# Kernel optimization log

Hardware: AMD Instinct MI355X
Metric: run time of the kernel (lower is better)

The kernel has to match this reference:

```python
import jax, jax.numpy as jnp
import numpy as np

N_NODES = 200000
H_DIM = 64
OUT_DIM = 32
NUM_RELS = 8
NUM_BASES = 8
N_EDGES = 1000000


def setup_inputs() -> dict:
    key = jax.random.key(0)
    ks = jax.random.split(key, 10)
    emb = jax.random.normal(ks[0], (N_NODES, H_DIM), dtype=jnp.float32) * 0.1
    basis1 = jax.random.normal(ks[1], (NUM_BASES, H_DIM, H_DIM), dtype=jnp.float32) * 0.05
    comp1 = jax.random.normal(ks[2], (NUM_RELS, NUM_BASES), dtype=jnp.float32)
    bias1 = jnp.zeros((H_DIM,), dtype=jnp.float32)
    basis2 = jax.random.normal(ks[3], (NUM_BASES, H_DIM, OUT_DIM), dtype=jnp.float32) * 0.05
    comp2 = jax.random.normal(ks[4], (NUM_RELS, NUM_BASES), dtype=jnp.float32)
    bias2 = jnp.zeros((OUT_DIM,), dtype=jnp.float32)
    src = jax.random.randint(ks[5], (N_EDGES,), 0, N_NODES, dtype=jnp.int32)
    dst = jax.random.randint(ks[6], (N_EDGES,), 0, N_NODES, dtype=jnp.int32)
    etype = jax.random.randint(ks[7], (N_EDGES,), 0, NUM_RELS, dtype=jnp.int32)
    norm = jax.random.uniform(ks[8], (N_EDGES, 1), dtype=jnp.float32)
    return {"emb": emb, "basis1": basis1, "comp1": comp1, "bias1": bias1,
            "basis2": basis2, "comp2": comp2, "bias2": bias2,
            "src": src, "dst": dst, "etype": etype, "norm": norm}


def _rel_graph_conv(x, basis, comp, bias, src, dst, etype, norm, num_nodes):
    # basis regularizer: W_r = sum_b comp[r,b] * basis[b]  -> [R, in, out]
    W = jnp.einsum('rb,bio->rio', comp, basis)
    # transform all nodes under every relation: [R, N, out]
    y = jnp.einsum('ni,rio->rno', x, W)
    # per-edge message: gather transformed src feature for the edge's relation
    msg = y[etype, src] * norm  # [E, out]
    # scatter-sum to destination nodes
    agg = jax.ops.segment_sum(msg, dst, num_segments=num_nodes)
    return agg + bias


def reference(emb, basis1, comp1, bias1, basis2, comp2, bias2, src, dst, etype, norm):
    h = _rel_graph_conv(emb, basis1, comp1, bias1, src, dst, etype, norm, emb.shape[0])
    h = _rel_graph_conv(h, basis2, comp2, bias2, src, dst, etype, norm, emb.shape[0])
    return h
```

## Files before the change

### kernel.cpp

```cpp
#include <hip/hip_runtime.h>
#include <hip/hip_bf16.h>

#define NRELS 8
#define NB 8
#define PBLK 256
#define BSH 9
#define BCAP 3584

typedef __attribute__((ext_vector_type(8))) short short8v;
typedef __attribute__((ext_vector_type(4))) float f32x4;

__device__ __forceinline__ short bfc(float f) {
    __hip_bfloat16 h = __float2bfloat16(f);
    return *reinterpret_cast<short*>(&h);
}
__device__ __forceinline__ float bf2f(ushort u) {
    return __uint_as_float((unsigned)u << 16);
}

__global__ void wprep_kernel(const float* __restrict__ basis1, const float* __restrict__ comp1,
                             const float* __restrict__ basis2, const float* __restrict__ comp2,
                             short* __restrict__ Wf1, short* __restrict__ Wf2) {
    int idx = blockIdx.x * blockDim.x + threadIdx.x;
    const int n1 = 16 * 4 * 64 * 8;
    const int n2 = 16 * 2 * 64 * 8;
    if (idx < n1) {
        int j = idx & 7, lane = (idx >> 3) & 63, nt = (idx >> 9) & 3, ks = idx >> 11;
        int k512 = ks * 32 + (lane >> 4) * 8 + j;
        int r = k512 >> 6, k64 = k512 & 63;
        int c = nt * 16 + (lane & 15);
        float s = 0.f;
#pragma unroll
        for (int b = 0; b < NB; ++b)
            s = fmaf(comp1[r * NB + b], basis1[b * 4096 + k64 * 64 + c], s);
        Wf1[idx] = bfc(s);
    } else if (idx < n1 + n2) {
        int i2 = idx - n1;
        int j = i2 & 7, lane = (i2 >> 3) & 63, nt = (i2 >> 9) & 1, ks = i2 >> 10;
        int k512 = ks * 32 + (lane >> 4) * 8 + j;
        int r = k512 >> 6, k64 = k512 & 63;
        int c = nt * 16 + (lane & 15);
        float s = 0.f;
#pragma unroll
        for (int b = 0; b < NB; ++b)
            s = fmaf(comp2[r * NB + b], basis2[b * 2048 + k64 * 32 + c], s);
        Wf2[i2] = bfc(s);
    }
}

__global__ void cvt_kernel(const float* __restrict__ in, ushort* __restrict__ outb, int n4) {
    for (int i = blockIdx.x * blockDim.x + threadIdx.x; i < n4;
         i += gridDim.x * blockDim.x) {
        float4 v = reinterpret_cast<const float4*>(in)[i];
        ushort4 o;
        o.x = (ushort)bfc(v.x); o.y = (ushort)bfc(v.y);
        o.z = (ushort)bfc(v.z); o.w = (ushort)bfc(v.w);
        reinterpret_cast<ushort4*>(outb)[i] = o;
    }
}

__global__ void histA_kernel(const int* __restrict__ dst, int* __restrict__ histM,
                             int nEdges, int nBuck, int chunk) {
    __shared__ int h[512];
    for (int t = threadIdx.x; t < nBuck; t += 256) h[t] = 0;
    __syncthreads();
    int start = blockIdx.x * chunk;
    int end = min(nEdges, start + chunk);
    for (int i = start + threadIdx.x; i < end; i += 256)
        atomicAdd(&h[dst[i] >> BSH], 1);
    __syncthreads();
    for (int t = threadIdx.x; t < nBuck; t += 256)
        histM[t * PBLK + blockIdx.x] = h[t];
}

__global__ void scanA_kernel(const int* __restrict__ histM, int* __restrict__ offs,
                             int* __restrict__ bucketBase, int nBuck, int nBlk, int nEdges) {
    __shared__ int tot[512];
    const int b = threadIdx.x;
    int s = 0;
    if (b < nBuck) {
        const int4* hp = (const int4*)(histM + b * nBlk);
        for (int k = 0; k < nBlk / 4; ++k) {
            int4 v = hp[k];
            s += v.x + v.y + v.z + v.w;
        }
    }
    tot[b] = s;
    __syncthreads();
    int own = s;
    for (int st = 1; st < 512; st <<= 1) {
        int t = (b >= st) ? tot[b - st] : 0;
        __syncthreads();
        tot[b] += t;
        __syncthreads();
    }
    int base = tot[b] - own;
    if (b < nBuck) {
        bucketBase[b] = base;
        int run = base;
        const int4* hp = (const int4*)(histM + b * nBlk);
        int4* op = (int4*)(offs + b * nBlk);
        for (int k = 0; k < nBlk / 4; ++k) {
            int4 h4 = hp[k];
            int4 o4;
            o4.x = run; run += h4.x;
            o4.y = run; run += h4.y;
            o4.z = run; run += h4.z;
            o4.w = run; run += h4.w;
            op[k] = o4;
        }
    }
    if (b == 0) bucketBase[nBuck] = nEdges;
}

__global__ void part_kernel(const int* __restrict__ src, const int* __restrict__ dst,
                            const int* __restrict__ et, const float* __restrict__ norm,
                            const int* __restrict__ offs, uint2* __restrict__ staged,
                            int nEdges, int nBuck, int chunk) {
    __shared__ int cur[512];
    for (int t = threadIdx.x; t < nBuck; t += 256)
        cur[t] = offs[t * PBLK + blockIdx.x];
    __syncthreads();
    int start = blockIdx.x * chunk;
    int end = min(nEdges, start + chunk);
    for (int i = start + threadIdx.x; i < end; i += 256) {
        int d = dst[i];
        int b = d >> BSH;
        int p = atomicAdd(&cur[b], 1);
        staged[p] = make_uint2(((unsigned)(d & 511) << 21) |
                               ((unsigned)src[i] << 3) | (unsigned)et[i],
                               __float_as_uint(norm[i]));
    }
}

__global__ void sortB_kernel(uint2* __restrict__ meta, const int* __restrict__ bucketBase,
                             int* __restrict__ endOff, int nNodes) {
    const int b = blockIdx.x;
    const int tid = threadIdx.x;
    const int e0 = bucketBase[b];
    const int n = min(bucketBase[b + 1] - e0, BCAP);
    __shared__ uint2 st[BCAP];
    __shared__ int h[4352];
    __shared__ int pb[256];
#pragma unroll
    for (int k = 0; k < 16; ++k) h[tid * 17 + k] = 0;
    __syncthreads();
    for (int j = tid; j < n; j += 256) {
        uint2 v = meta[e0 + j];
        st[j] = v;
        int key = (int)((v.x >> 21) << 3) | (int)(v.x & 7u);
        atomicAdd(&h[key + (key >> 4)], 1);
    }
    __syncthreads();
    int loc[16];
    int s = 0;
#pragma unroll
    for (int k = 0; k < 16; ++k) { loc[k] = h[tid * 17 + k]; s += loc[k]; }
    pb[tid] = s;
    __syncthreads();
    for (int stp = 1; stp < 256; stp <<= 1) {
        int t = (tid >= stp) ? pb[tid - stp] : 0;
        __syncthreads();
        pb[tid] += t;
        __syncthreads();
    }
    int run = pb[tid] - s;
    const int d0 = b << BSH;
#pragma unroll
    for (int k = 0; k < 16; ++k) {
        h[tid * 17 + k] = run;
        run += loc[k];
        if ((k & 7) == 7) {
            int d = d0 + tid * 2 + (k >> 3);
            if (d < nNodes) endOff[d] = e0 + run;
        }
    }
    __syncthreads();
    for (int j = tid; j < n; j += 256) {
        uint2 v = st[j];
        int key = (int)((v.x >> 21) << 3) | (int)(v.x & 7u);
        int r = atomicAdd(&h[key + (key >> 4)], 1);
        meta[e0 + r] = make_uint2(v.x & 0x1FFFFFu, v.y);
    }
}

template <int OUT, typename OutT>
__global__ __launch_bounds__(256, 4) void fused_kernel(
    const ushort* __restrict__ xb, const short* __restrict__ Wf,
    const uint2* __restrict__ meta, const int* __restrict__ endOff,
    const float* __restrict__ bias, OutT* __restrict__ out, int nNodes) {
    constexpr int NT = OUT / 16;
    __shared__ ushort ab[16][520];
    const int lane = threadIdx.x & 63;
    const int wslot = threadIdx.x >> 6;
    const int d0blk = blockIdx.x * 16;
    const int d0 = d0blk + wslot * 4;
    const int rowBase = wslot * 4;

    {
        ushort4 z4 = {0, 0, 0, 0};
#pragma unroll
        for (int r = 0; r < 4; ++r) {
            *(ushort4*)&ab[rowBase + r][lane * 4] = z4;
            *(ushort4*)&ab[rowBase + r][256 + lane * 4] = z4;
        }
    }

    if (d0 < nNodes) {
        const int d1 = min(d0 + 4, nNodes);
        int bndv = 0x7fffffff;
        if (lane < 4) bndv = endOff[min(d0 + lane, nNodes - 1)];
        const int eEnd = __builtin_amdgcn_readlane(bndv, d1 - 1 - d0);
        int e = __builtin_amdgcn_readfirstlane((d0 == 0) ? 0 : endOff[d0 - 1]);
        int dl = 0;
        int bnd = __builtin_amdgcn_readlane(bndv, 0);
        float acc = 0.f;
        int curRel = -1;

        auto flushRel = [&]() {
            if (curRel >= 0) {
                ab[rowBase + dl][curRel * 64 + lane] = (ushort)bfc(acc);
                acc = 0.f;
            }
            curRel = -1;
        };
        auto nextDst = [&]() {
            flushRel();
            ++dl;
            bnd = __builtin_amdgcn_readlane(bndv, min(dl, 3));
        };
        auto gx = [&](unsigned key) -> ushort {
            return xb[(size_t)(key >> 3) * 64 + lane];
        };
        auto consume = [&](uint2 M, ushort xv_) {
            while (e >= bnd) nextDst();
            int r = (int)(M.x & 7u);
            if (r != curRel) { flushRel(); curRel = r; }
            acc = fmaf(__uint_as_float(M.y), bf2f(xv_), acc);
            ++e;
        };

        if (e < eEnd) {
            const int eL = eEnd - 1;
            uint2 Ma[8], Mb[8];
            ushort Va[8];
#pragma unroll
            for (int k = 0; k < 8; ++k) Ma[k] = meta[min(e + k, eL)];
#pragma unroll
            for (int k = 0; k < 8; ++k) Mb[k] = meta[min(e + 8 + k, eL)];
#pragma unroll
            for (int k = 0; k < 8; ++k) Va[k] = gx(Ma[k].x);

            const int nFull = (eEnd - e) >> 3;
            for (int blk = 0; blk < nFull; ++blk) {
                ushort Vb[8];
                uint2 Mc[8];
#pragma unroll
                for (int k = 0; k < 8; ++k) Vb[k] = gx(Mb[k].x);
#pragma unroll
                for (int k = 0; k < 8; ++k) Mc[k] = meta[min(e + 16 + k, eL)];
#pragma unroll
                for (int k = 0; k < 8; ++k) consume(Ma[k], Va[k]);
#pragma unroll
                for (int k = 0; k < 8; ++k) { Ma[k] = Mb[k]; Mb[k] = Mc[k]; Va[k] = Vb[k]; }
            }
            const int rem = eEnd - e;
#pragma unroll
            for (int k = 0; k < 8; ++k)
                if (k < rem) consume(Ma[k], Va[k]);
        }
        while (dl < 4) nextDst();
    }
    __syncthreads();

    if (wslot < NT) {
        const int ml = lane & 15, kg = lane >> 4;
        const int nt = wslot;
        f32x4 acc4 = (f32x4){0.f, 0.f, 0.f, 0.f};
#pragma unroll
        for (int ks = 0; ks < 16; ++ks) {
            short8v A = *(const short8v*)&ab[ml][ks * 32 + kg * 8];
            short8v B = *(const short8v*)(Wf + ((size_t)(ks * NT + nt) * 64 + lane) * 8);
            acc4 = __builtin_amdgcn_mfma_f32_16x16x32_bf16(A, B, acc4, 0, 0, 0);
        }
        float bvv = bias[nt * 16 + ml];
#pragma unroll
        for (int i = 0; i < 4; ++i) {
            int d = d0blk + kg * 4 + i;
            if (d < nNodes) {
                float v = acc4[i] + bvv;
                if constexpr (sizeof(OutT) == 2)
                    out[(size_t)d * OUT + nt * 16 + ml] = (OutT)(ushort)bfc(v);
                else
                    out[(size_t)d * OUT + nt * 16 + ml] = (OutT)v;
            }
        }
    }
}

extern "C" void kernel_launch(void* const* d_in, const int* in_sizes, int n_in,
                              void* d_out, int out_size, void* d_ws, size_t ws_size,
                              hipStream_t stream) {
    const float* emb    = (const float*)d_in[0];
    const float* basis1 = (const float*)d_in[1];
    const float* comp1  = (const float*)d_in[2];
    const float* bias1  = (const float*)d_in[3];
    const float* basis2 = (const float*)d_in[4];
    const float* comp2  = (const float*)d_in[5];
    const float* bias2  = (const float*)d_in[6];
    const int*   src    = (const int*)d_in[7];
    const int*   dst    = (const int*)d_in[8];
    const int*   etype  = (const int*)d_in[9];
    const float* norm   = (const float*)d_in[10];
    float* out = (float*)d_out;

    const int nNodes = in_sizes[0] / 64;
    const int nEdges = in_sizes[7];

    const int nBuck = (nNodes + 511) >> BSH;
    const int chunk = (nEdges + PBLK - 1) / PBLK;

    char* ws = (char*)d_ws;
    short* Wf1        = (short*)(ws);
    short* Wf2        = (short*)(ws + 65536);
    int*   histM      = (int*)(ws + 98304);
    int*   offs       = (int*)(ws + 498688);
    int*   bucketBase = (int*)(ws + 899072);
    int*   endOff     = (int*)(ws + 900640);
    size_t offMeta = 1703936;
    uint2* meta       = (uint2*)(ws + offMeta);
    size_t offX = offMeta + (size_t)nEdges * 8;
    ushort* embb = (ushort*)(ws + offX);
    ushort* h1b  = (ushort*)(ws + offX + (size_t)nNodes * 64 * 2);

    wprep_kernel<<<192, 256, 0, stream>>>(basis1, comp1, basis2, comp2, Wf1, Wf2);
    cvt_kernel<<<1024, 256, 0, stream>>>(emb, embb, nNodes * 16);
    histA_kernel<<<PBLK, 256, 0, stream>>>(dst, histM, nEdges, nBuck, chunk);
    scanA_kernel<<<1, 512, 0, stream>>>(histM, offs, bucketBase, nBuck, PBLK, nEdges);
    part_kernel<<<PBLK, 256, 0, stream>>>(src, dst, etype, norm, offs, meta,
                                          nEdges, nBuck, chunk);
    sortB_kernel<<<nBuck, 256, 0, stream>>>(meta, bucketBase, endOff, nNodes);

    const int fBlocks = (nNodes + 15) / 16;
    fused_kernel<64, ushort><<<fBlocks, 256, 0, stream>>>(
        embb, Wf1, meta, endOff, bias1, h1b, nNodes);
    fused_kernel<32, float><<<fBlocks, 256, 0, stream>>>(
        h1b, Wf2, meta, endOff, bias2, out, nNodes);
}
```

Measured before the change: 211.4 us.

## Merge preprocessing kernels and use 8 waves of 2 nodes per fused block

The small preprocessing kernels (histogram, bf16 conversion, scan, weight prep) are merged into two launches, with the embedding conversion split across both so it runs alongside the histogram and the scan. Fewer launches and less serialization in the short setup phase are the goal. The fused aggregation kernel now runs 512 threads per block, each wave handling 2 destination nodes instead of 4. This gives more waves for latency hiding on the irregular gathers, at the cost of more blocks-worth of register pressure under the new launch bounds and idle waves in the MFMA phase.

```diff
diff --git a/kernel.cpp b/kernel.cpp
--- a/kernel.cpp
+++ b/kernel.cpp
@@ -18,10 +18,12 @@
     return __uint_as_float((unsigned)u << 16);
 }
 
-__global__ void wprep_kernel(const float* __restrict__ basis1, const float* __restrict__ comp1,
-                             const float* __restrict__ basis2, const float* __restrict__ comp2,
-                             short* __restrict__ Wf1, short* __restrict__ Wf2) {
-    int idx = blockIdx.x * blockDim.x + threadIdx.x;
+__device__ __forceinline__ void wprep_body(const float* __restrict__ basis1,
+                                           const float* __restrict__ comp1,
+                                           const float* __restrict__ basis2,
+                                           const float* __restrict__ comp2,
+                                           short* __restrict__ Wf1, short* __restrict__ Wf2,
+                                           int idx) {
     const int n1 = 16 * 4 * 64 * 8;
     const int n2 = 16 * 2 * 64 * 8;
     if (idx < n1) {
@@ -48,33 +50,32 @@
     }
 }
 
-__global__ void cvt_kernel(const float* __restrict__ in, ushort* __restrict__ outb, int n4) {
-    for (int i = blockIdx.x * blockDim.x + threadIdx.x; i < n4;
-         i += gridDim.x * blockDim.x) {
-        float4 v = reinterpret_cast<const float4*>(in)[i];
-        ushort4 o;
-        o.x = (ushort)bfc(v.x); o.y = (ushort)bfc(v.y);
-        o.z = (ushort)bfc(v.z); o.w = (ushort)bfc(v.w);
-        reinterpret_cast<ushort4*>(outb)[i] = o;
-    }
-}
-
-__global__ void histA_kernel(const int* __restrict__ dst, int* __restrict__ histM,
-                             int nEdges, int nBuck, int chunk) {
+__device__ __forceinline__ void cvt4(const float* __restrict__ in, ushort* __restrict__ outb,
+                                     int i) {
+    float4 v = reinterpret_cast<const float4*>(in)[i];
+    ushort4 o;
+    o.x = (ushort)bfc(v.x); o.y = (ushort)bfc(v.y);
+    o.z = (ushort)bfc(v.z); o.w = (ushort)bfc(v.w);
+    reinterpret_cast<ushort4*>(outb)[i] = o;
+}
+
+__device__ __forceinline__ void histA_body(const int* __restrict__ dst, int* __restrict__ histM,
+                                           int nEdges, int nBuck, int chunk, int bid) {
     __shared__ int h[512];
     for (int t = threadIdx.x; t < nBuck; t += 256) h[t] = 0;
     __syncthreads();
-    int start = blockIdx.x * chunk;
+    int start = bid * chunk;
     int end = min(nEdges, start + chunk);
     for (int i = start + threadIdx.x; i < end; i += 256)
         atomicAdd(&h[dst[i] >> BSH], 1);
     __syncthreads();
     for (int t = threadIdx.x; t < nBuck; t += 256)
-        histM[t * PBLK + blockIdx.x] = h[t];
-}
-
-__global__ void scanA_kernel(const int* __restrict__ histM, int* __restrict__ offs,
-                             int* __restrict__ bucketBase, int nBuck, int nBlk, int nEdges) {
+        histM[t * PBLK + bid] = h[t];
+}
+
+__device__ __forceinline__ void scanA_body(const int* __restrict__ histM, int* __restrict__ offs,
+                                           int* __restrict__ bucketBase, int nBuck, int nBlk,
+                                           int nEdges) {
     __shared__ int tot[512];
     const int b = threadIdx.x;
     int s = 0;
@@ -85,16 +86,16 @@
             s += v.x + v.y + v.z + v.w;
         }
     }
-    tot[b] = s;
+    if (b < 512) tot[b] = s;
     __syncthreads();
     int own = s;
     for (int st = 1; st < 512; st <<= 1) {
-        int t = (b >= st) ? tot[b - st] : 0;
+        int t = (b >= st && b < 512) ? tot[b - st] : 0;
         __syncthreads();
-        tot[b] += t;
+        if (b < 512) tot[b] += t;
         __syncthreads();
     }
-    int base = tot[b] - own;
+    int base = (b < 512) ? (tot[b] - own) : 0;
     if (b < nBuck) {
         bucketBase[b] = base;
         int run = base;
@@ -113,6 +114,39 @@
     if (b == 0) bucketBase[nBuck] = nEdges;
 }
 
+__global__ __launch_bounds__(256) void p1_kernel(
+    const int* __restrict__ dst, int* __restrict__ histM, int nEdges, int nBuck, int chunk,
+    const float* __restrict__ in, ushort* __restrict__ outb, int n4h, int cvtBlocks) {
+    if ((int)blockIdx.x < PBLK) {
+        histA_body(dst, histM, nEdges, nBuck, chunk, blockIdx.x);
+        return;
+    }
+    int w = (int)blockIdx.x - PBLK;
+    for (int i = w * 256 + threadIdx.x; i < n4h; i += cvtBlocks * 256)
+        cvt4(in, outb, i);
+}
+
+__global__ __launch_bounds__(512) void p2_kernel(
+    const int* __restrict__ histM, int* __restrict__ offs, int* __restrict__ bucketBase,
+    int nBuck, int nEdges,
+    const float* __restrict__ basis1, const float* __restrict__ comp1,
+    const float* __restrict__ basis2, const float* __restrict__ comp2,
+    short* __restrict__ Wf1, short* __restrict__ Wf2,
+    const float* __restrict__ in, ushort* __restrict__ outb, int n4h, int n4, int cvtBlocks) {
+    if (blockIdx.x == 0) {
+        scanA_body(histM, offs, bucketBase, nBuck, PBLK, nEdges);
+        return;
+    }
+    if ((int)blockIdx.x <= 96) {
+        wprep_body(basis1, comp1, basis2, comp2, Wf1, Wf2,
+                   ((int)blockIdx.x - 1) * 512 + (int)threadIdx.x);
+        return;
+    }
+    int w = (int)blockIdx.x - 97;
+    for (int i = n4h + w * 512 + threadIdx.x; i < n4; i += cvtBlocks * 512)
+        cvt4(in, outb, i);
+}
+
 __global__ void part_kernel(const int* __restrict__ src, const int* __restrict__ dst,
                             const int* __restrict__ et, const float* __restrict__ norm,
                             const int* __restrict__ offs, uint2* __restrict__ staged,
@@ -185,7 +219,7 @@
 }
 
 template <int OUT, typename OutT>
-__global__ __launch_bounds__(256, 4) void fused_kernel(
+__global__ __launch_bounds__(512, 8) void fused_kernel(
     const ushort* __restrict__ xb, const short* __restrict__ Wf,
     const uint2* __restrict__ meta, const int* __restrict__ endOff,
     const float* __restrict__ bias, OutT* __restrict__ out, int nNodes) {
@@ -194,22 +228,22 @@
     const int lane = threadIdx.x & 63;
     const int wslot = threadIdx.x >> 6;
     const int d0blk = blockIdx.x * 16;
-    const int d0 = d0blk + wslot * 4;
-    const int rowBase = wslot * 4;
+    const int d0 = d0blk + wslot * 2;
+    const int rowBase = wslot * 2;
 
     {
         ushort4 z4 = {0, 0, 0, 0};
 #pragma unroll
-        for (int r = 0; r < 4; ++r) {
+        for (int r = 0; r < 2; ++r) {
             *(ushort4*)&ab[rowBase + r][lane * 4] = z4;
             *(ushort4*)&ab[rowBase + r][256 + lane * 4] = z4;
         }
     }
 
     if (d0 < nNodes) {
-        const int d1 = min(d0 + 4, nNodes);
+        const int d1 = min(d0 + 2, nNodes);
         int bndv = 0x7fffffff;
-        if (lane < 4) bndv = endOff[min(d0 + lane, nNodes - 1)];
+        if (lane < 2) bndv = endOff[min(d0 + lane, nNodes - 1)];
         const int eEnd = __builtin_amdgcn_readlane(bndv, d1 - 1 - d0);
         int e = __builtin_amdgcn_readfirstlane((d0 == 0) ? 0 : endOff[d0 - 1]);
         int dl = 0;
@@ -227,7 +261,7 @@
         auto nextDst = [&]() {
             flushRel();
             ++dl;
-            bnd = __builtin_amdgcn_readlane(bndv, min(dl, 3));
+            bnd = __builtin_amdgcn_readlane(bndv, min(dl, 1));
         };
         auto gx = [&](unsigned key) -> ushort {
             return xb[(size_t)(key >> 3) * 64 + lane];
@@ -269,7 +303,7 @@
             for (int k = 0; k < 8; ++k)
                 if (k < rem) consume(Ma[k], Va[k]);
         }
-        while (dl < 4) nextDst();
+        while (dl < 2) nextDst();
     }
     __syncthreads();
 
@@ -333,17 +367,21 @@
     ushort* embb = (ushort*)(ws + offX);
     ushort* h1b  = (ushort*)(ws + offX + (size_t)nNodes * 64 * 2);
 
-    wprep_kernel<<<192, 256, 0, stream>>>(basis1, comp1, basis2, comp2, Wf1, Wf2);
-    cvt_kernel<<<1024, 256, 0, stream>>>(emb, embb, nNodes * 16);
-    histA_kernel<<<PBLK, 256, 0, stream>>>(dst, histM, nEdges, nBuck, chunk);
-    scanA_kernel<<<1, 512, 0, stream>>>(histM, offs, bucketBase, nBuck, PBLK, nEdges);
+    const int n4 = nNodes * 16;
+    const int n4h = n4 / 2;
+
+    p1_kernel<<<PBLK + 768, 256, 0, stream>>>(dst, histM, nEdges, nBuck, chunk,
+                                              emb, embb, n4h, 768);
+    p2_kernel<<<1 + 96 + 512, 512, 0, stream>>>(histM, offs, bucketBase, nBuck, nEdges,
+                                                basis1, comp1, basis2, comp2, Wf1, Wf2,
+                                                emb, embb, n4h, n4, 512);
     part_kernel<<<PBLK, 256, 0, stream>>>(src, dst, etype, norm, offs, meta,
                                           nEdges, nBuck, chunk);
     sortB_kernel<<<nBuck, 256, 0, stream>>>(meta, bucketBase, endOff, nNodes);
 
     const int fBlocks = (nNodes + 15) / 16;
-    fused_kernel<64, ushort><<<fBlocks, 256, 0, stream>>>(
+    fused_kernel<64, ushort><<<fBlocks, 512, 0, stream>>>(
         embb, Wf1, meta, endOff, bias1, h1b, nNodes);
-    fused_kernel<32, float><<<fBlocks, 256, 0, stream>>>(
+    fused_kernel<32, float><<<fBlocks, 512, 0, stream>>>(
         h1b, Wf2, meta, endOff, bias2, out, nNodes);
 }
```

Measured after the change: 233.1 us. 10.2% more time.
